# Kernel tuning notes

Measured on AMD Instinct MI355X. Metric: run time of the kernel, lower is better.

The kernel has to match this reference:

```python
import jax, jax.numpy as jnp
import numpy as np

B, T, D = 2, 2048, 1024
N, H = 16, 64  # num_heads, head_dim
LOG2E = 1.442695041
NEG_INF = -1.0e9


def setup_inputs() -> dict:
    key = jax.random.key(0)
    ks = jax.random.split(key, 6)
    return {
        "input_tensor": jax.random.normal(ks[0], (B, T, D), dtype=jnp.float32),
        "attention_mask": jax.random.randint(ks[1], (B, 1, T, T), 0, 2, dtype=jnp.int32),
        "wq": jax.random.normal(ks[2], (D, N, H), dtype=jnp.float32),
        "bq": jnp.zeros((N, H), dtype=jnp.float32),
        "wk": jax.random.normal(ks[3], (D, N, H), dtype=jnp.float32),
        "bk": jnp.zeros((N, H), dtype=jnp.float32),
        "wv": jax.random.normal(ks[4], (D, N, H), dtype=jnp.float32),
        "bv": jnp.zeros((N, H), dtype=jnp.float32),
        "wo": jax.random.normal(ks[5], (D, N, H), dtype=jnp.float32),
        "bo": jnp.zeros((D,), dtype=jnp.float32),
        "per_dim_scale": jnp.zeros((H,), dtype=jnp.float32),
    }


def reference(input_tensor, attention_mask, wq, bq, wk, bk, wv, bv, wo, bo, per_dim_scale):
    # QKV projections: [B,T,D] x [D,N,H] -> [B,T,N,H]
    q = jnp.einsum('btd,dnh->btnh', input_tensor, wq) + bq
    k = jnp.einsum('btd,dnh->btnh', input_tensor, wk) + bk
    v = jnp.einsum('btd,dnh->btnh', input_tensor, wv) + bv
    # per-dim query scaling: (log2(e)/sqrt(H)) * softplus(per_dim_scale)
    scale = (LOG2E / jnp.sqrt(jnp.asarray(H, q.dtype))) * jax.nn.softplus(per_dim_scale)
    q = q * scale
    # scores: [B,N,T,S]
    scores = jnp.einsum('btnh,bsnh->bnts', q, k)
    scores = jnp.where(attention_mask == 0, jnp.asarray(NEG_INF, scores.dtype), scores)
    weights = jax.nn.softmax(scores, axis=-1)
    # AV: [B,N,T,S] x [B,S,N,H] -> [B,T,N,H]
    attn_out = jnp.einsum('bnts,bsnh->btnh', weights, v)
    # output projection: [B,T,N,H] x [D,N,H] -> [B,T,D]
    return jnp.einsum('btnh,dnh->btd', attn_out, wo) + bo
```

## Files before the change

kernel.cpp:

```cpp
#include <hip/hip_runtime.h>
#include <math.h>

typedef __bf16 bf16;
typedef __attribute__((ext_vector_type(8))) __bf16 bf16x8;
typedef __attribute__((ext_vector_type(4))) __bf16 bf16x4;
typedef __attribute__((ext_vector_type(4))) float f32x4;

#define BB 2
#define TT 2048
#define DD 1024
#define NHD 16
#define HD 64
#define MM (BB*TT)
#define LOG2E_F 1.442695041f
#define NEGINF_F (-1.0e9f)

__device__ __forceinline__ void gld16(const bf16* g, bf16* l)
{
    __builtin_amdgcn_global_load_lds(
        (const __attribute__((address_space(1))) unsigned int*)g,
        (__attribute__((address_space(3))) unsigned int*)l, 16, 0, 0);
}

__global__ __launch_bounds__(256)
void prep_all(const float* __restrict__ X, const int* __restrict__ m,
              const float* __restrict__ wq, const float* __restrict__ wk,
              const float* __restrict__ wv, const float* __restrict__ wo,
              bf16* __restrict__ Xh, bf16* __restrict__ Xl,
              bf16* __restrict__ qkh, bf16* __restrict__ qkl,
              bf16* __restrict__ vh, bf16* __restrict__ ob,
              bf16* __restrict__ madd)
{
    __shared__ float tile[32][33];
    const int bid = blockIdx.x;
    const int t   = threadIdx.x;

    if (bid < 4096) {
        int i = bid * 256 + t;
        float4 v = ((const float4*)X)[i];
        float f[4] = {v.x, v.y, v.z, v.w};
        bf16x4 h, l;
        #pragma unroll
        for (int j = 0; j < 4; ++j) {
            bf16 hh = (bf16)f[j];
            h[j] = hh;
            l[j] = (bf16)(f[j] - (float)hh);
        }
        *(bf16x4*)(Xh + (size_t)i * 4) = h;
        *(bf16x4*)(Xl + (size_t)i * 4) = l;
        return;
    }
    if (bid < 8192) {
        const int idx = bid - 4096;
        const int z   = idx >> 10;
        const int bx  = (idx & 31) << 5;
        const int by  = ((idx >> 5) & 31) << 5;
        const int r   = t >> 3;
        const int c4  = (t & 7) << 2;
        if (z == 3) {
            float4 v = *(const float4*)(wo + (size_t)(by + r) * 1024 + bx + c4);
            bf16x4 o = { (bf16)v.x, (bf16)v.y, (bf16)v.z, (bf16)v.w };
            *(bf16x4*)(ob + (size_t)(by + r) * 1024 + bx + c4) = o;
            return;
        }
        const float* src = (z == 0) ? wq : ((z == 1) ? wk : wv);
        bf16* oh = (z == 0) ? qkh : ((z == 1) ? qkh + 1048576 : vh);
        bf16* ol = (z == 0) ? qkl : ((z == 1) ? qkl + 1048576 : nullptr);
        float4 v = *(const float4*)(src + (size_t)(by + r) * 1024 + bx + c4);
        tile[r][c4+0] = v.x; tile[r][c4+1] = v.y;
        tile[r][c4+2] = v.z; tile[r][c4+3] = v.w;
        __syncthreads();
        bf16x4 hv, lv;
        #pragma unroll
        for (int j = 0; j < 4; ++j) {
            float f = tile[c4 + j][r];
            bf16 h = (bf16)f;
            hv[j] = h;
            lv[j] = (bf16)(f - (float)h);
        }
        *(bf16x4*)(oh + (size_t)(bx + r) * 1024 + by + c4) = hv;
        if (ol)
            *(bf16x4*)(ol + (size_t)(bx + r) * 1024 + by + c4) = lv;
        return;
    }
    {
        int i = (bid - 8192) * 256 + t;
        const int4* mp = (const int4*)m + (size_t)i * 2;
        int4 a  = mp[0];
        int4 b4 = mp[1];
        bf16x8 o;
        o[0] = (bf16)(a.x  ? 0.f : NEGINF_F);
        o[1] = (bf16)(a.y  ? 0.f : NEGINF_F);
        o[2] = (bf16)(a.z  ? 0.f : NEGINF_F);
        o[3] = (bf16)(a.w  ? 0.f : NEGINF_F);
        o[4] = (bf16)(b4.x ? 0.f : NEGINF_F);
        o[5] = (bf16)(b4.y ? 0.f : NEGINF_F);
        o[6] = (bf16)(b4.z ? 0.f : NEGINF_F);
        o[7] = (bf16)(b4.w ? 0.f : NEGINF_F);
        *(bf16x8*)(madd + (size_t)i * 8) = o;
    }
}

__global__ __launch_bounds__(256)
void gemm_proj(const bf16* __restrict__ Xh, const bf16* __restrict__ Xl,
               const bf16* __restrict__ Wh, const bf16* __restrict__ Wl,
               const bf16* __restrict__ Wvh,
               const float* __restrict__ bq, const float* __restrict__ bk,
               const float* __restrict__ bv, const float* __restrict__ pds,
               bf16* __restrict__ oQh, bf16* __restrict__ oQl,
               bf16* __restrict__ oKh, bf16* __restrict__ oKl,
               bf16* __restrict__ oVt)
{
    __shared__ bf16 S[4][128 * 32];

    int bid = blockIdx.x;
    if (bid < 512) bid = ((bid & 7) << 6) + (bid >> 3);
    else {
        int idx = bid - 512;
        bid = 512 + (((idx & 7) << 5) + (idx >> 3));
    }

    const int t    = threadIdx.x;
    const int lane = t & 63;
    const int w    = t >> 6;
    const int quad = lane >> 4, l15 = lane & 15;
    const int wm   = (w >> 1) << 6;
    const int wn   = (w & 1)  << 6;

    const int jr0 = ((w * 2 + 0) << 4) + (lane >> 2);
    const int jr1 = ((w * 2 + 1) << 4) + (lane >> 2);
    const int kch = (lane & 3) << 3;
    const int off0 = (w * 2 + 0) * 512;
    const int off1 = (w * 2 + 1) * 512;

    if (bid < 512) {
        const int m0 = (bid >> 4) << 7;
        const int n0 = (bid & 15) << 7;
        bf16* Ah = S[0]; bf16* Al = S[1]; bf16* Bh = S[2]; bf16* Bl = S[3];

        const bf16* pAh0 = Xh + (size_t)(m0 + jr0) * DD + kch;
        const bf16* pAh1 = Xh + (size_t)(m0 + jr1) * DD + kch;
        const bf16* pAl0 = Xl + (size_t)(m0 + jr0) * DD + kch;
        const bf16* pAl1 = Xl + (size_t)(m0 + jr1) * DD + kch;
        const bf16* pBh0 = Wh + (size_t)(n0 + jr0) * DD + kch;
        const bf16* pBh1 = Wh + (size_t)(n0 + jr1) * DD + kch;
        const bf16* pBl0 = Wl + (size_t)(n0 + jr0) * DD + kch;
        const bf16* pBl1 = Wl + (size_t)(n0 + jr1) * DD + kch;

        f32x4 acc[4][4] = {};

        for (int k0 = 0; k0 < DD; k0 += 32) {
            __syncthreads();
            gld16(pAh0 + k0, Ah + off0);  gld16(pAh1 + k0, Ah + off1);
            gld16(pAl0 + k0, Al + off0);  gld16(pAl1 + k0, Al + off1);
            gld16(pBh0 + k0, Bh + off0);  gld16(pBh1 + k0, Bh + off1);
            gld16(pBl0 + k0, Bl + off0);  gld16(pBl1 + k0, Bl + off1);
            __syncthreads();

            bf16x8 ah[4], bh[4];
            #pragma unroll
            for (int mt = 0; mt < 4; ++mt)
                ah[mt] = *(const bf16x8*)(Ah + (wm + (mt << 4) + l15) * 32 + (quad << 3));
            #pragma unroll
            for (int nt = 0; nt < 4; ++nt)
                bh[nt] = *(const bf16x8*)(Bh + (wn + (nt << 4) + l15) * 32 + (quad << 3));
            #pragma unroll
            for (int mt = 0; mt < 4; ++mt)
                #pragma unroll
                for (int nt = 0; nt < 4; ++nt)
                    acc[mt][nt] = __builtin_amdgcn_mfma_f32_16x16x32_bf16(
                        ah[mt], bh[nt], acc[mt][nt], 0, 0, 0);

            bf16x8 bl[4];
            #pragma unroll
            for (int nt = 0; nt < 4; ++nt)
                bl[nt] = *(const bf16x8*)(Bl + (wn + (nt << 4) + l15) * 32 + (quad << 3));
            #pragma unroll
            for (int mt = 0; mt < 4; ++mt)
                #pragma unroll
                for (int nt = 0; nt < 4; ++nt)
                    acc[mt][nt] = __builtin_amdgcn_mfma_f32_16x16x32_bf16(
                        ah[mt], bl[nt], acc[mt][nt], 0, 0, 0);

            bf16x8 al[4];
            #pragma unroll
            for (int mt = 0; mt < 4; ++mt)
                al[mt] = *(const bf16x8*)(Al + (wm + (mt << 4) + l15) * 32 + (quad << 3));
            #pragma unroll
            for (int mt = 0; mt < 4; ++mt)
                #pragma unroll
                for (int nt = 0; nt < 4; ++nt)
                    acc[mt][nt] = __builtin_amdgcn_mfma_f32_16x16x32_bf16(
                        al[mt], bh[nt], acc[mt][nt], 0, 0, 0);
        }

        #pragma unroll
        for (int nt = 0; nt < 4; ++nt) {
            const int col = n0 + wn + (nt << 4) + l15;
            const int isQ = (col < 1024);
            const int nh  = col & 1023;
            const int n   = nh >> 6, h = nh & 63;
            const float bcol = isQ ? bq[nh] : bk[nh];
            float s = 1.f;
            if (isQ) {
                float x  = pds[h];
                float sp = fmaxf(x, 0.f) + log1pf(expf(-fabsf(x)));
                s = (LOG2E_F * LOG2E_F / 8.0f) * sp;
            }
            bf16* dH = isQ ? oQh : oKh;
            bf16* dL = isQ ? oQl : oKl;
            #pragma unroll
            for (int mt = 0; mt < 4; ++mt) {
                #pragma unroll
                for (int reg = 0; reg < 4; ++reg) {
                    const int row = m0 + wm + (mt << 4) + (quad << 2) + reg;
                    const int bi  = row >> 11;
                    const int tt  = row & (TT - 1);
                    float val = (acc[mt][nt][reg] + bcol) * s;
                    const size_t idx = (((size_t)bi * NHD + n) * TT + tt) * HD + h;
                    bf16 hi = (bf16)val;
                    dH[idx] = hi;
                    dL[idx] = (bf16)(val - (float)hi);
                }
            }
        }
    } else {
        const int idx = bid - 512;
        const int m0  = (idx >> 5) << 7;
        const int n0  = (idx & 31) << 7;
        bf16* As = S[0]; bf16* Bs = S[2];

        const bf16* Ap0 = Wvh + (size_t)(m0 + jr0) * DD + kch;
        const bf16* Ap1 = Wvh + (size_t)(m0 + jr1) * DD + kch;
        const bf16* Bp0 = Xh  + (size_t)(n0 + jr0) * DD + kch;
        const bf16* Bp1 = Xh  + (size_t)(n0 + jr1) * DD + kch;

        f32x4 acc[4][4] = {};

        for (int k0 = 0; k0 < DD; k0 += 32) {
            __syncthreads();
            gld16(Ap0 + k0, As + off0);
            gld16(Ap1 + k0, As + off1);
            gld16(Bp0 + k0, Bs + off0);
            gld16(Bp1 + k0, Bs + off1);
            __syncthreads();
            bf16x8 af[4], bfm[4];
            #pragma unroll
            for (int mt = 0; mt < 4; ++mt)
                af[mt] = *(const bf16x8*)(As + (wm + (mt << 4) + l15) * 32 + (quad << 3));
            #pragma unroll
            for (int nt = 0; nt < 4; ++nt)
                bfm[nt] = *(const bf16x8*)(Bs + (wn + (nt << 4) + l15) * 32 + (quad << 3));
            #pragma unroll
            for (int mt = 0; mt < 4; ++mt)
                #pragma unroll
                for (int nt = 0; nt < 4; ++nt)
                    acc[mt][nt] = __builtin_amdgcn_mfma_f32_16x16x32_bf16(
                        af[mt], bfm[nt], acc[mt][nt], 0, 0, 0);
        }

        #pragma unroll
        for (int nt = 0; nt < 4; ++nt) {
            const int col = n0 + wn + (nt << 4) + l15;
            const int bi  = col >> 11;
            const int tt  = col & (TT - 1);
            #pragma unroll
            for (int mt = 0; mt < 4; ++mt) {
                #pragma unroll
                for (int reg = 0; reg < 4; ++reg) {
                    const int row = m0 + wm + (mt << 4) + (quad << 2) + reg;
                    float val = acc[mt][nt][reg] + bv[row];
                    oVt[((size_t)bi * 1024 + row) * TT + tt] = (bf16)val;
                }
            }
        }
    }
}

__global__ __launch_bounds__(256)
void gemm_out(const bf16* __restrict__ A, const bf16* __restrict__ Bt,
              const float* __restrict__ bias, float* __restrict__ oF)
{
    __shared__ bf16 As[128 * 32];
    __shared__ bf16 Bs[64 * 32];

    const int t    = threadIdx.x;
    const int lane = t & 63;
    const int w    = t >> 6;
    const int quad = lane >> 4, l15 = lane & 15;
    const int m0   = blockIdx.y << 7;
    const int n0   = blockIdx.x << 6;
    const int wm   = (w >> 1) << 6;
    const int wn   = (w & 1)  << 5;

    const int jr0 = ((w * 2 + 0) << 4) + (lane >> 2);
    const int jr1 = ((w * 2 + 1) << 4) + (lane >> 2);
    const int jrB = (w << 4) + (lane >> 2);
    const int kch = (lane & 3) << 3;

    bf16* lA0 = As + (w * 2 + 0) * 512;
    bf16* lA1 = As + (w * 2 + 1) * 512;
    bf16* lB  = Bs + w * 512;

    const bf16* Ap0 = A  + (size_t)(m0 + jr0) * DD + kch;
    const bf16* Ap1 = A  + (size_t)(m0 + jr1) * DD + kch;
    const bf16* Bp  = Bt + (size_t)(n0 + jrB) * DD + kch;

    f32x4 acc[4][2] = {};

    for (int k0 = 0; k0 < DD; k0 += 32) {
        __syncthreads();
        gld16(Ap0 + k0, lA0);
        gld16(Ap1 + k0, lA1);
        gld16(Bp + k0, lB);
        __syncthreads();
        bf16x8 af[4], bfm[2];
        #pragma unroll
        for (int mt = 0; mt < 4; ++mt)
            af[mt] = *(const bf16x8*)(As + (wm + (mt << 4) + l15) * 32 + (quad << 3));
        #pragma unroll
        for (int nt = 0; nt < 2; ++nt)
            bfm[nt] = *(const bf16x8*)(Bs + (wn + (nt << 4) + l15) * 32 + (quad << 3));
        #pragma unroll
        for (int mt = 0; mt < 4; ++mt)
            #pragma unroll
            for (int nt = 0; nt < 2; ++nt)
                acc[mt][nt] = __builtin_amdgcn_mfma_f32_16x16x32_bf16(
                    af[mt], bfm[nt], acc[mt][nt], 0, 0, 0);
    }

    #pragma unroll
    for (int nt = 0; nt < 2; ++nt) {
        const int col = n0 + wn + (nt << 4) + l15;
        const float bcol = bias[col];
        #pragma unroll
        for (int mt = 0; mt < 4; ++mt) {
            #pragma unroll
            for (int reg = 0; reg < 4; ++reg) {
                const int row = m0 + wm + (mt << 4) + (quad << 2) + reg;
                oF[(size_t)row * DD + col] = acc[mt][nt][reg] + bcol;
            }
        }
    }
}

__global__ __launch_bounds__(512)
void attn_mfma(const bf16* __restrict__ Qh, const bf16* __restrict__ Ql,
               const bf16* __restrict__ Kh, const bf16* __restrict__ Kl,
               const bf16* __restrict__ Vt,
               const bf16* __restrict__ Madd,
               bf16* __restrict__ AO)
{
    __shared__ bf16 Ksh[64 * 64];
    __shared__ bf16 Ksl[64 * 64];
    __shared__ bf16 Vts[64 * 64];
    __shared__ bf16 PS [8][16 * 64];

    const int t    = threadIdx.x;
    const int lane = t & 63;
    const int w    = t >> 6;
    const int quad = lane >> 4, l15 = lane & 15;
    const int bn   = blockIdx.y;
    const int b    = bn >> 4, n = bn & 15;
    const int q0   = blockIdx.x << 7;

    const bf16* Qbh = Qh + (size_t)bn * TT * HD;
    const bf16* Qbl = Ql + (size_t)bn * TT * HD;
    const bf16* Kbh = Kh + (size_t)bn * TT * HD;
    const bf16* Kbl = Kl + (size_t)bn * TT * HD;
    const bf16* Vtb = Vt + (size_t)bn * HD * TT;
    const bf16* Mb  = Madd + (size_t)b * TT * TT;

    const int qrow = q0 + (w << 4) + l15;
    bf16x8 qfh[2], qfl[2];
    qfh[0] = *(const bf16x8*)(Qbh + (size_t)qrow * HD + (quad << 3));
    qfh[1] = *(const bf16x8*)(Qbh + (size_t)qrow * HD + 32 + (quad << 3));
    qfl[0] = *(const bf16x8*)(Qbl + (size_t)qrow * HD + (quad << 3));
    qfl[1] = *(const bf16x8*)(Qbl + (size_t)qrow * HD + 32 + (quad << 3));

    f32x4 O[4];
    #pragma unroll
    for (int i = 0; i < 4; ++i) O[i] = (f32x4){0.f,0.f,0.f,0.f};
    f32x4 Ol = (f32x4){0.f,0.f,0.f,0.f};
    float m_i = -INFINITY;

    const bf16 onev = (bf16)1.0f;
    const bf16x8 ones = { onev, onev, onev, onev, onev, onev, onev, onev };

    const int rS = t >> 3;
    const int cG = (t & 7) << 3;
    const int cL = (((t & 7) ^ (rS & 7)) << 3);
    const int sw8 = (l15 & 7) << 3;

    const bf16* mrow0 = Mb + (size_t)qrow * TT + (quad << 2);

    for (int kb = 0; kb < TT; kb += 64) {
        bf16x8 khv = *(const bf16x8*)(Kbh + (size_t)(kb + rS) * HD + cG);
        bf16x8 klv = *(const bf16x8*)(Kbl + (size_t)(kb + rS) * HD + cG);
        bf16x8 vv  = *(const bf16x8*)(Vtb + (size_t)rS * TT + kb + cG);
        const bf16* mr = mrow0 + kb;
        ushort4 mu0 = *(const ushort4*)(mr);
        ushort4 mu1 = *(const ushort4*)(mr + 16);
        ushort4 mu2 = *(const ushort4*)(mr + 32);
        ushort4 mu3 = *(const ushort4*)(mr + 48);

        __syncthreads();
        *(bf16x8*)&Ksh[rS * 64 + cL] = khv;
        *(bf16x8*)&Ksl[rS * 64 + cL] = klv;
        *(bf16x8*)&Vts[rS * 64 + cL] = vv;
        __syncthreads();

        f32x4 s_acc[4];
        s_acc[0][0] = __uint_as_float((unsigned)mu0.x << 16);
        s_acc[0][1] = __uint_as_float((unsigned)mu0.y << 16);
        s_acc[0][2] = __uint_as_float((unsigned)mu0.z << 16);
        s_acc[0][3] = __uint_as_float((unsigned)mu0.w << 16);
        s_acc[1][0] = __uint_as_float((unsigned)mu1.x << 16);
        s_acc[1][1] = __uint_as_float((unsigned)mu1.y << 16);
        s_acc[1][2] = __uint_as_float((unsigned)mu1.z << 16);
        s_acc[1][3] = __uint_as_float((unsigned)mu1.w << 16);
        s_acc[2][0] = __uint_as_float((unsigned)mu2.x << 16);
        s_acc[2][1] = __uint_as_float((unsigned)mu2.y << 16);
        s_acc[2][2] = __uint_as_float((unsigned)mu2.z << 16);
        s_acc[2][3] = __uint_as_float((unsigned)mu2.w << 16);
        s_acc[3][0] = __uint_as_float((unsigned)mu3.x << 16);
        s_acc[3][1] = __uint_as_float((unsigned)mu3.y << 16);
        s_acc[3][2] = __uint_as_float((unsigned)mu3.z << 16);
        s_acc[3][3] = __uint_as_float((unsigned)mu3.w << 16);

        __builtin_amdgcn_s_setprio(1);
        #pragma unroll
        for (int k2 = 0; k2 < 2; ++k2) {
            #pragma unroll
            for (int nt = 0; nt < 4; ++nt) {
                const int ro = ((nt << 4) + l15) * 64;
                const int co = ((k2 << 5) + (quad << 3)) ^ sw8;
                bf16x8 bkh = *(const bf16x8*)&Ksh[ro + co];
                bf16x8 bkl = *(const bf16x8*)&Ksl[ro + co];
                s_acc[nt] = __builtin_amdgcn_mfma_f32_16x16x32_bf16(bkh, qfh[k2], s_acc[nt], 0, 0, 0);
                s_acc[nt] = __builtin_amdgcn_mfma_f32_16x16x32_bf16(bkl, qfh[k2], s_acc[nt], 0, 0, 0);
                s_acc[nt] = __builtin_amdgcn_mfma_f32_16x16x32_bf16(bkh, qfl[k2], s_acc[nt], 0, 0, 0);
            }
        }
        __builtin_amdgcn_s_setprio(0);

        float t0 = fmaxf(fmaxf(s_acc[0][0], s_acc[0][1]), s_acc[0][2]);
        float t1 = fmaxf(fmaxf(s_acc[0][3], s_acc[1][0]), s_acc[1][1]);
        float t2 = fmaxf(fmaxf(s_acc[1][2], s_acc[1][3]), s_acc[2][0]);
        float t3 = fmaxf(fmaxf(s_acc[2][1], s_acc[2][2]), s_acc[2][3]);
        float t4 = fmaxf(fmaxf(s_acc[3][0], s_acc[3][1]), s_acc[3][2]);
        float mx = fmaxf(fmaxf(fmaxf(t0, t1), t2),
                         fmaxf(fmaxf(t3, t4), s_acc[3][3]));
        mx = fmaxf(mx, __shfl_xor(mx, 16));
        mx = fmaxf(mx, __shfl_xor(mx, 32));

        if (!__all(mx <= m_i + 8.0f)) {
            const float mnew  = fmaxf(m_i, mx);
            const float alpha = exp2f(m_i - mnew);
            #pragma unroll
            for (int nt = 0; nt < 4; ++nt) {
                O[nt][0] *= alpha; O[nt][1] *= alpha;
                O[nt][2] *= alpha; O[nt][3] *= alpha;
            }
            Ol[0] *= alpha; Ol[1] *= alpha; Ol[2] *= alpha; Ol[3] *= alpha;
            m_i = mnew;
        }

        float p[16];
        #pragma unroll
        for (int nt = 0; nt < 4; ++nt)
            #pragma unroll
            for (int reg = 0; reg < 4; ++reg)
                p[nt * 4 + reg] = exp2f(s_acc[nt][reg] - m_i);

        #pragma unroll
        for (int nt = 0; nt < 4; ++nt) {
            bf16x4 pv = { (bf16)p[nt * 4 + 0], (bf16)p[nt * 4 + 1],
                          (bf16)p[nt * 4 + 2], (bf16)p[nt * 4 + 3] };
            *(bf16x4*)&PS[w][l15 * 64 + (((nt << 4) + (quad << 2)) ^ sw8)] = pv;
        }

        __builtin_amdgcn_s_setprio(1);
        #pragma unroll
        for (int s2i = 0; s2i < 2; ++s2i) {
            bf16x8 ap = *(const bf16x8*)&PS[w][l15 * 64 + (((s2i << 5) + (quad << 3)) ^ sw8)];
            Ol = __builtin_amdgcn_mfma_f32_16x16x32_bf16(ones, ap, Ol, 0, 0, 0);
            #pragma unroll
            for (int nt = 0; nt < 4; ++nt) {
                bf16x8 bv = *(const bf16x8*)&Vts[((nt << 4) + l15) * 64
                                                 + (((s2i << 5) + (quad << 3)) ^ sw8)];
                O[nt] = __builtin_amdgcn_mfma_f32_16x16x32_bf16(bv, ap, O[nt], 0, 0, 0);
            }
        }
        __builtin_amdgcn_s_setprio(0);
    }

    {
        const float inv = 1.0f / Ol[0];
        const size_t base = ((size_t)b * TT + qrow) * (NHD * HD) + (size_t)n * HD;
        #pragma unroll
        for (int nt = 0; nt < 4; ++nt) {
            bf16x4 o = { (bf16)(O[nt][0] * inv), (bf16)(O[nt][1] * inv),
                         (bf16)(O[nt][2] * inv), (bf16)(O[nt][3] * inv) };
            *(bf16x4*)(AO + base + (nt << 4) + (quad << 2)) = o;
        }
    }
}

extern "C" void kernel_launch(void* const* d_in, const int* in_sizes, int n_in,
                              void* d_out, int out_size, void* d_ws, size_t ws_size,
                              hipStream_t stream)
{
    const float* X   = (const float*)d_in[0];
    const int*   msk = (const int*)d_in[1];
    const float* wq  = (const float*)d_in[2];
    const float* bq  = (const float*)d_in[3];
    const float* wk  = (const float*)d_in[4];
    const float* bk  = (const float*)d_in[5];
    const float* wv  = (const float*)d_in[6];
    const float* bv  = (const float*)d_in[7];
    const float* wo  = (const float*)d_in[8];
    const float* bo  = (const float*)d_in[9];
    const float* pds = (const float*)d_in[10];
    float* out = (float*)d_out;

    bf16* ws   = (bf16*)d_ws;
    bf16* Xh   = ws;
    bf16* Xl   = ws + 4194304;
    bf16* WQKh = ws + 8388608;
    bf16* WQKl = ws + 10485760;
    bf16* Wvh  = ws + 12582912;
    bf16* Wob  = ws + 13631488;
    bf16* Qhb  = ws + 14680064;
    bf16* Qlb  = ws + 18874368;
    bf16* Khb  = ws + 23068672;
    bf16* Klb  = ws + 27262976;
    bf16* Vtb  = ws + 32505856;
    bf16* AOb  = Xh;
    bf16* madd = (bf16*)d_out;

    dim3 blk(256);

    prep_all<<<12288, blk, 0, stream>>>(X, msk, wq, wk, wv, wo,
                                        Xh, Xl, WQKh, WQKl, Wvh, Wob, madd);

    gemm_proj<<<768, blk, 0, stream>>>(
        Xh, Xl, WQKh, WQKl, Wvh, bq, bk, bv, pds,
        Qhb, Qlb, Khb, Klb, Vtb);

    dim3 ga(TT / 128, BB * NHD);
    attn_mfma<<<ga, dim3(512), 0, stream>>>(
        Qhb, Qlb, Khb, Klb, Vtb, madd, AOb);

    gemm_out<<<dim3(16, 32), blk, 0, stream>>>(AOb, Wob, bo, out);
}
```

Before: 305.7 us.

## Double-buffer K/V tiles in attention kernel with register prefetch

Restructures the attention loop so that the next K/V/mask tile is loaded from global memory into registers while the current tile is being computed from shared memory. The tile is then written into the alternate LDS buffer, and each iteration needs only one barrier instead of two. It also adds a min-blocks hint of 4 to the launch bounds. In exchange, LDS use and register pressure go up, which could force spills or reduce occupancy.

After: 304.8 us. Within noise of the previous version (-0.3%).

```diff
diff --git a/kernel.cpp b/kernel.cpp
--- a/kernel.cpp
+++ b/kernel.cpp
@@ -344,17 +344,17 @@
     }
 }
 
-__global__ __launch_bounds__(512)
+__global__ __launch_bounds__(512, 4)
 void attn_mfma(const bf16* __restrict__ Qh, const bf16* __restrict__ Ql,
                const bf16* __restrict__ Kh, const bf16* __restrict__ Kl,
                const bf16* __restrict__ Vt,
                const bf16* __restrict__ Madd,
                bf16* __restrict__ AO)
 {
-    __shared__ bf16 Ksh[64 * 64];
-    __shared__ bf16 Ksl[64 * 64];
-    __shared__ bf16 Vts[64 * 64];
-    __shared__ bf16 PS [8][16 * 64];
+    __shared__ bf16 KH[2][64 * 64];
+    __shared__ bf16 KL[2][64 * 64];
+    __shared__ bf16 VS[2][64 * 64];
+    __shared__ bf16 PS[8][16 * 64];
 
     const int t    = threadIdx.x;
     const int lane = t & 63;
@@ -394,21 +394,40 @@
 
     const bf16* mrow0 = Mb + (size_t)qrow * TT + (quad << 2);
 
-    for (int kb = 0; kb < TT; kb += 64) {
-        bf16x8 khv = *(const bf16x8*)(Kbh + (size_t)(kb + rS) * HD + cG);
-        bf16x8 klv = *(const bf16x8*)(Kbl + (size_t)(kb + rS) * HD + cG);
-        bf16x8 vv  = *(const bf16x8*)(Vtb + (size_t)rS * TT + kb + cG);
-        const bf16* mr = mrow0 + kb;
-        ushort4 mu0 = *(const ushort4*)(mr);
-        ushort4 mu1 = *(const ushort4*)(mr + 16);
-        ushort4 mu2 = *(const ushort4*)(mr + 32);
-        ushort4 mu3 = *(const ushort4*)(mr + 48);
-
-        __syncthreads();
-        *(bf16x8*)&Ksh[rS * 64 + cL] = khv;
-        *(bf16x8*)&Ksl[rS * 64 + cL] = klv;
-        *(bf16x8*)&Vts[rS * 64 + cL] = vv;
-        __syncthreads();
+    {
+        bf16x8 khv = *(const bf16x8*)(Kbh + (size_t)rS * HD + cG);
+        bf16x8 klv = *(const bf16x8*)(Kbl + (size_t)rS * HD + cG);
+        bf16x8 vv  = *(const bf16x8*)(Vtb + (size_t)rS * TT + cG);
+        *(bf16x8*)&KH[0][rS * 64 + cL] = khv;
+        *(bf16x8*)&KL[0][rS * 64 + cL] = klv;
+        *(bf16x8*)&VS[0][rS * 64 + cL] = vv;
+    }
+    ushort4 mu0 = *(const ushort4*)(mrow0);
+    ushort4 mu1 = *(const ushort4*)(mrow0 + 16);
+    ushort4 mu2 = *(const ushort4*)(mrow0 + 32);
+    ushort4 mu3 = *(const ushort4*)(mrow0 + 48);
+    __syncthreads();
+
+    int cur = 0;
+    for (int it = 0; it < 32; ++it) {
+        const int last = (it == 31);
+        bf16x8 nkh, nkl, nvv;
+        ushort4 nm0, nm1, nm2, nm3;
+        if (!last) {
+            const int kb2 = (it + 1) << 6;
+            nkh = *(const bf16x8*)(Kbh + (size_t)(kb2 + rS) * HD + cG);
+            nkl = *(const bf16x8*)(Kbl + (size_t)(kb2 + rS) * HD + cG);
+            nvv = *(const bf16x8*)(Vtb + (size_t)rS * TT + kb2 + cG);
+            const bf16* mr = mrow0 + kb2;
+            nm0 = *(const ushort4*)(mr);
+            nm1 = *(const ushort4*)(mr + 16);
+            nm2 = *(const ushort4*)(mr + 32);
+            nm3 = *(const ushort4*)(mr + 48);
+        }
+
+        const bf16* curKH = &KH[cur][0];
+        const bf16* curKL = &KL[cur][0];
+        const bf16* curVS = &VS[cur][0];
 
         f32x4 s_acc[4];
         s_acc[0][0] = __uint_as_float((unsigned)mu0.x << 16);
@@ -435,8 +454,8 @@
             for (int nt = 0; nt < 4; ++nt) {
                 const int ro = ((nt << 4) + l15) * 64;
                 const int co = ((k2 << 5) + (quad << 3)) ^ sw8;
-                bf16x8 bkh = *(const bf16x8*)&Ksh[ro + co];
-                bf16x8 bkl = *(const bf16x8*)&Ksl[ro + co];
+                bf16x8 bkh = *(const bf16x8*)&curKH[ro + co];
+                bf16x8 bkl = *(const bf16x8*)&curKL[ro + co];
                 s_acc[nt] = __builtin_amdgcn_mfma_f32_16x16x32_bf16(bkh, qfh[k2], s_acc[nt], 0, 0, 0);
                 s_acc[nt] = __builtin_amdgcn_mfma_f32_16x16x32_bf16(bkl, qfh[k2], s_acc[nt], 0, 0, 0);
                 s_acc[nt] = __builtin_amdgcn_mfma_f32_16x16x32_bf16(bkh, qfl[k2], s_acc[nt], 0, 0, 0);
@@ -487,12 +506,22 @@
             Ol = __builtin_amdgcn_mfma_f32_16x16x32_bf16(ones, ap, Ol, 0, 0, 0);
             #pragma unroll
             for (int nt = 0; nt < 4; ++nt) {
-                bf16x8 bv = *(const bf16x8*)&Vts[((nt << 4) + l15) * 64
-                                                 + (((s2i << 5) + (quad << 3)) ^ sw8)];
+                bf16x8 bv = *(const bf16x8*)&curVS[((nt << 4) + l15) * 64
+                                                   + (((s2i << 5) + (quad << 3)) ^ sw8)];
                 O[nt] = __builtin_amdgcn_mfma_f32_16x16x32_bf16(bv, ap, O[nt], 0, 0, 0);
             }
         }
         __builtin_amdgcn_s_setprio(0);
+
+        if (!last) {
+            const int nxt = cur ^ 1;
+            *(bf16x8*)&KH[nxt][rS * 64 + cL] = nkh;
+            *(bf16x8*)&KL[nxt][rS * 64 + cL] = nkl;
+            *(bf16x8*)&VS[nxt][rS * 64 + cL] = nvv;
+            mu0 = nm0; mu1 = nm1; mu2 = nm2; mu3 = nm3;
+            __syncthreads();
+            cur = nxt;
+        }
     }
 
     {
```
